# Performance work log

Measured on AMD Instinct MI355X. Metric: run time of the kernel, lower is better.

## Reference

```python
import jax, jax.numpy as jnp
import numpy as np

B, HOP, D = 32768, 32, 64  # batch, hop_number (neighbor samples), embed dim (ent == rel)


def setup_inputs() -> dict:
    key = jax.random.key(0)
    ks = jax.random.split(key, 7)
    s = 0.1  # mimic glorot-scale init for weights
    return {
        "entity": jax.random.normal(ks[0], (B, 1, D), dtype=jnp.float32),
        "relation": jax.random.normal(ks[1], (B, HOP, D), dtype=jnp.float32),
        "neighbor": jax.random.normal(ks[2], (B, HOP, D), dtype=jnp.float32),
        "w_h": jax.random.normal(ks[3], (D, D), dtype=jnp.float32) * s,
        "w_t": jax.random.normal(ks[4], (D, D), dtype=jnp.float32) * s,
        "w_r": jax.random.normal(ks[5], (D, D), dtype=jnp.float32) * s,
        "v_a": jax.random.normal(ks[6], (3 * D, 1), dtype=jnp.float32) * s,
    }


def reference(entity, relation, neighbor, w_h, w_t, w_r, v_a):
    # entity: (B,1,D); relation/neighbor: (B,HOP,D)
    b, hop, _ = relation.shape
    # f_entity = zeros_like(relation[:,:,0]).reshape(-1, hop, 1)  -> all zeros
    f_entity = jnp.zeros((b, hop, 1), dtype=relation.dtype)
    # K.batch_dot(f_entity, entity, [2,1]): (B,HOP,1)x(B,1,D) -> (B,HOP,D) (zeros)
    entity_hat = jnp.einsum('bhi,bid->bhd', f_entity, entity)
    head_entity = entity_hat @ w_h            # (B,HOP,D)
    rel = relation @ w_r                      # (B,HOP,D)
    tail_entity = neighbor @ w_t              # (B,HOP,D)
    head_rel_tail = jnp.concatenate([head_entity, rel, tail_entity], axis=-1)  # (B,HOP,3D)
    scores = jnp.tanh(head_rel_tail) @ v_a    # (B,HOP,1)
    return jax.nn.softmax(scores, axis=-2)    # softmax over hop axis
```

## Files before the change

### kernel.cpp

```cpp
#include <hip/hip_runtime.h>


typedef short bf16x8 __attribute__((ext_vector_type(8)));
typedef float f32x4 __attribute__((ext_vector_type(4)));

#define NB   32768
#define NHOP 32
#define ND   64

__device__ __forceinline__ float tanh_fast(float x) {
  float cx = fminf(fmaxf(x, -20.f), 20.f);
  float e2 = __expf(2.f * cx);
  return (e2 - 1.f) * __builtin_amdgcn_rcpf(e2 + 1.f);
}

__device__ __forceinline__ void split2(float4 v0, float4 v1, bf16x8 &hi, bf16x8 &lo) {
  float xs[8] = {v0.x, v0.y, v0.z, v0.w, v1.x, v1.y, v1.z, v1.w};
#pragma unroll
  for (int j = 0; j < 8; ++j) {
    unsigned u = __builtin_bit_cast(unsigned, xs[j]);
    hi[j] = (short)(u >> 16);
    float hif = __builtin_bit_cast(float, u & 0xffff0000u);
    lo[j] = (short)(__builtin_bit_cast(unsigned, xs[j] - hif) >> 16);
  }
}

__global__ __launch_bounds__(256, 2)
void attn_fused(const float* __restrict__ rel, const float* __restrict__ nbr,
                const float* __restrict__ wr, const float* __restrict__ wt,
                const float* __restrict__ va, float* __restrict__ out, int nwaves) {
  const int lane = threadIdx.x & 63;
  const int wid  = (blockIdx.x * blockDim.x + threadIdx.x) >> 6;
  const int l15  = lane & 15;
  const int lg   = lane >> 4;

  bf16x8 wf[2][2][4][2];
#pragma unroll
  for (int mat = 0; mat < 2; ++mat) {
    const float* W = mat ? wt : wr;
#pragma unroll
    for (int c = 0; c < 2; ++c)
#pragma unroll
      for (int nt = 0; nt < 4; ++nt) {
        bf16x8 hi, lo;
#pragma unroll
        for (int j = 0; j < 8; ++j) {
          float x = W[(c * 32 + lg * 8 + j) * 64 + nt * 16 + l15];
          unsigned u = __builtin_bit_cast(unsigned, x);
          hi[j] = (short)(u >> 16);
          float hif = __builtin_bit_cast(float, u & 0xffff0000u);
          lo[j] = (short)(__builtin_bit_cast(unsigned, x - hif) >> 16);
        }
        wf[mat][c][nt][0] = hi;
        wf[mat][c][nt][1] = lo;
      }
  }

  float va1[4], va2[4];
#pragma unroll
  for (int nt = 0; nt < 4; ++nt) {
    va1[nt] = va[64 + nt * 16 + l15];
    va2[nt] = va[128 + nt * 16 + l15];
  }

  for (int b = wid; b < NB; b += nwaves) {
    float sc[2][4];
#pragma unroll
    for (int tt = 0; tt < 2; ++tt) {
      const size_t row = (size_t)b * NHOP + tt * 16 + l15;
      const float* rbase = rel + row * ND + lg * 8;
      const float* tbase = nbr + row * ND + lg * 8;
      float4 r0 = *(const float4*)(rbase);
      float4 r1 = *(const float4*)(rbase + 4);
      float4 r2 = *(const float4*)(rbase + 32);
      float4 r3 = *(const float4*)(rbase + 36);
      float4 t0 = *(const float4*)(tbase);
      float4 t1 = *(const float4*)(tbase + 4);
      float4 t2 = *(const float4*)(tbase + 32);
      float4 t3 = *(const float4*)(tbase + 36);

      f32x4 part = {0.f, 0.f, 0.f, 0.f};

      {
        bf16x8 ahi[2], alo[2];
        split2(r0, r1, ahi[0], alo[0]);
        split2(r2, r3, ahi[1], alo[1]);
        f32x4 acc[4];
#pragma unroll
        for (int nt = 0; nt < 4; ++nt) acc[nt] = (f32x4){0.f, 0.f, 0.f, 0.f};
#pragma unroll
        for (int c = 0; c < 2; ++c)
#pragma unroll
          for (int nt = 0; nt < 4; ++nt) {
            acc[nt] = __builtin_amdgcn_mfma_f32_16x16x32_bf16(ahi[c], wf[0][c][nt][0], acc[nt], 0, 0, 0);
            acc[nt] = __builtin_amdgcn_mfma_f32_16x16x32_bf16(alo[c], wf[0][c][nt][0], acc[nt], 0, 0, 0);
            acc[nt] = __builtin_amdgcn_mfma_f32_16x16x32_bf16(ahi[c], wf[0][c][nt][1], acc[nt], 0, 0, 0);
          }
#pragma unroll
        for (int nt = 0; nt < 4; ++nt)
#pragma unroll
          for (int rr = 0; rr < 4; ++rr)
            part[rr] += tanh_fast(acc[nt][rr]) * va1[nt];
      }

      {
        bf16x8 ahi[2], alo[2];
        split2(t0, t1, ahi[0], alo[0]);
        split2(t2, t3, ahi[1], alo[1]);
        f32x4 acc[4];
#pragma unroll
        for (int nt = 0; nt < 4; ++nt) acc[nt] = (f32x4){0.f, 0.f, 0.f, 0.f};
#pragma unroll
        for (int c = 0; c < 2; ++c)
#pragma unroll
          for (int nt = 0; nt < 4; ++nt) {
            acc[nt] = __builtin_amdgcn_mfma_f32_16x16x32_bf16(ahi[c], wf[1][c][nt][0], acc[nt], 0, 0, 0);
            acc[nt] = __builtin_amdgcn_mfma_f32_16x16x32_bf16(alo[c], wf[1][c][nt][0], acc[nt], 0, 0, 0);
            acc[nt] = __builtin_amdgcn_mfma_f32_16x16x32_bf16(ahi[c], wf[1][c][nt][1], acc[nt], 0, 0, 0);
          }
#pragma unroll
        for (int nt = 0; nt < 4; ++nt)
#pragma unroll
          for (int rr = 0; rr < 4; ++rr)
            part[rr] += tanh_fast(acc[nt][rr]) * va2[nt];
      }

#pragma unroll
      for (int m = 1; m <= 8; m <<= 1)
#pragma unroll
        for (int rr = 0; rr < 4; ++rr)
          part[rr] += __shfl_xor(part[rr], m, 64);
#pragma unroll
      for (int rr = 0; rr < 4; ++rr) sc[tt][rr] = part[rr];
    }

    float smax = fmaxf(fmaxf(sc[0][0], sc[0][1]), fmaxf(sc[0][2], sc[0][3]));
    smax = fmaxf(smax, fmaxf(fmaxf(sc[1][0], sc[1][1]), fmaxf(sc[1][2], sc[1][3])));
    smax = fmaxf(smax, __shfl_xor(smax, 16, 64));
    smax = fmaxf(smax, __shfl_xor(smax, 32, 64));

    float e[2][4];
    float ssum = 0.f;
#pragma unroll
    for (int tt = 0; tt < 2; ++tt)
#pragma unroll
      for (int rr = 0; rr < 4; ++rr) {
        e[tt][rr] = __expf(sc[tt][rr] - smax);
        ssum += e[tt][rr];
      }
    ssum += __shfl_xor(ssum, 16, 64);
    ssum += __shfl_xor(ssum, 32, 64);
    float inv = __builtin_amdgcn_rcpf(ssum);

    if (l15 == 0) {
      float* ob = out + (size_t)b * NHOP;
      float4 o0 = {e[0][0] * inv, e[0][1] * inv, e[0][2] * inv, e[0][3] * inv};
      float4 o1 = {e[1][0] * inv, e[1][1] * inv, e[1][2] * inv, e[1][3] * inv};
      *(float4*)(ob + lg * 4)      = o0;
      *(float4*)(ob + 16 + lg * 4) = o1;
    }
  }
}

extern "C" void kernel_launch(void* const* d_in, const int* in_sizes, int n_in,
                              void* d_out, int out_size, void* d_ws, size_t ws_size,
                              hipStream_t stream) {
  const float* rel = (const float*)d_in[1];
  const float* nbr = (const float*)d_in[2];
  const float* wt  = (const float*)d_in[4];
  const float* wr  = (const float*)d_in[5];
  const float* va  = (const float*)d_in[6];
  float* out = (float*)d_out;

  const int blocks = 1024;
  attn_fused<<<blocks, 256, 0, stream>>>(rel, nbr, wr, wt, va, out, blocks * 4);
}
```

Baseline: 534.5 us.

## Stage split weights in LDS, software-pipeline loads, cheaper tanh, more blocks

Weight hi/lo bf16 fragments are now built cooperatively once per block into shared memory instead of being held per-wave in registers. This frees VGPRs, so occupancy goes to 3 blocks per CU and the grid grows to 2048 blocks. The main loop prefetches the next batch's relation tile while the neighbor half is computed, and the two hop tiles now share each weight-fragment load. tanh uses a cheaper exp2/rcp form without clamping, and split2 packs its outputs with perm instructions. The cost is extra LDS reads per MFMA group and one block-level barrier.

After: 623.7 us. +16.7%, slower.

```diff
diff --git a/kernel.cpp b/kernel.cpp
--- a/kernel.cpp
+++ b/kernel.cpp
@@ -3,58 +3,48 @@
 
 typedef short bf16x8 __attribute__((ext_vector_type(8)));
 typedef float f32x4 __attribute__((ext_vector_type(4)));
+typedef unsigned int u32x4 __attribute__((ext_vector_type(4)));
 
 #define NB   32768
 #define NHOP 32
 #define ND   64
+#define NBLK 2048
+#define NWAVES (NBLK * 4)
 
-__device__ __forceinline__ float tanh_fast(float x) {
-  float cx = fminf(fmaxf(x, -20.f), 20.f);
-  float e2 = __expf(2.f * cx);
-  return (e2 - 1.f) * __builtin_amdgcn_rcpf(e2 + 1.f);
+__device__ __forceinline__ float tanh_cheap(float x) {
+  float e2 = exp2f(x * 2.885390081777927f);
+  return fmaf(-2.f, __builtin_amdgcn_rcpf(e2 + 1.f), 1.f);
 }
 
 __device__ __forceinline__ void split2(float4 v0, float4 v1, bf16x8 &hi, bf16x8 &lo) {
   float xs[8] = {v0.x, v0.y, v0.z, v0.w, v1.x, v1.y, v1.z, v1.w};
+  u32x4 hw, lw;
 #pragma unroll
-  for (int j = 0; j < 8; ++j) {
-    unsigned u = __builtin_bit_cast(unsigned, xs[j]);
-    hi[j] = (short)(u >> 16);
-    float hif = __builtin_bit_cast(float, u & 0xffff0000u);
-    lo[j] = (short)(__builtin_bit_cast(unsigned, xs[j] - hif) >> 16);
+  for (int p = 0; p < 4; ++p) {
+    unsigned ub = __builtin_bit_cast(unsigned, xs[2 * p]);
+    unsigned ua = __builtin_bit_cast(unsigned, xs[2 * p + 1]);
+    hw[p] = __builtin_amdgcn_perm(ua, ub, 0x07060302u);
+    float hb = __builtin_bit_cast(float, ub & 0xffff0000u);
+    float ha = __builtin_bit_cast(float, ua & 0xffff0000u);
+    unsigned lb = __builtin_bit_cast(unsigned, xs[2 * p] - hb);
+    unsigned la = __builtin_bit_cast(unsigned, xs[2 * p + 1] - ha);
+    lw[p] = __builtin_amdgcn_perm(la, lb, 0x07060302u);
   }
+  hi = __builtin_bit_cast(bf16x8, hw);
+  lo = __builtin_bit_cast(bf16x8, lw);
 }
 
-__global__ __launch_bounds__(256, 2)
+__global__ __launch_bounds__(256, 3)
 void attn_fused(const float* __restrict__ rel, const float* __restrict__ nbr,
                 const float* __restrict__ wr, const float* __restrict__ wt,
-                const float* __restrict__ va, float* __restrict__ out, int nwaves) {
-  const int lane = threadIdx.x & 63;
-  const int wid  = (blockIdx.x * blockDim.x + threadIdx.x) >> 6;
-  const int l15  = lane & 15;
-  const int lg   = lane >> 4;
+                const float* __restrict__ va, float* __restrict__ out) {
+  __shared__ bf16x8 wsl[32][64];
 
-  bf16x8 wf[2][2][4][2];
-#pragma unroll
-  for (int mat = 0; mat < 2; ++mat) {
-    const float* W = mat ? wt : wr;
-#pragma unroll
-    for (int c = 0; c < 2; ++c)
-#pragma unroll
-      for (int nt = 0; nt < 4; ++nt) {
-        bf16x8 hi, lo;
-#pragma unroll
-        for (int j = 0; j < 8; ++j) {
-          float x = W[(c * 32 + lg * 8 + j) * 64 + nt * 16 + l15];
-          unsigned u = __builtin_bit_cast(unsigned, x);
-          hi[j] = (short)(u >> 16);
-          float hif = __builtin_bit_cast(float, u & 0xffff0000u);
-          lo[j] = (short)(__builtin_bit_cast(unsigned, x - hif) >> 16);
-        }
-        wf[mat][c][nt][0] = hi;
-        wf[mat][c][nt][1] = lo;
-      }
-  }
+  const int lane  = threadIdx.x & 63;
+  const int wslot = threadIdx.x >> 6;
+  const int wid   = (int)blockIdx.x * 4 + wslot;
+  const int l15   = lane & 15;
+  const int lg    = lane >> 4;
 
   float va1[4], va2[4];
 #pragma unroll
@@ -63,76 +53,100 @@
     va2[nt] = va[128 + nt * 16 + l15];
   }
 
-  for (int b = wid; b < NB; b += nwaves) {
-    float sc[2][4];
-#pragma unroll
-    for (int tt = 0; tt < 2; ++tt) {
-      const size_t row = (size_t)b * NHOP + tt * 16 + l15;
-      const float* rbase = rel + row * ND + lg * 8;
-      const float* tbase = nbr + row * ND + lg * 8;
-      float4 r0 = *(const float4*)(rbase);
-      float4 r1 = *(const float4*)(rbase + 4);
-      float4 r2 = *(const float4*)(rbase + 32);
-      float4 r3 = *(const float4*)(rbase + 36);
-      float4 t0 = *(const float4*)(tbase);
-      float4 t1 = *(const float4*)(tbase + 4);
-      float4 t2 = *(const float4*)(tbase + 32);
-      float4 t3 = *(const float4*)(tbase + 36);
+#define LOADM(DST, SRC, B) do {                                           \
+    const float* _p0 = (SRC) + ((size_t)(B) * NHOP + l15) * ND + lg * 8;  \
+    DST[0][0] = *(const float4*)(_p0);                                    \
+    DST[0][1] = *(const float4*)(_p0 + 4);                                \
+    DST[0][2] = *(const float4*)(_p0 + 32);                               \
+    DST[0][3] = *(const float4*)(_p0 + 36);                               \
+    const float* _p1 = _p0 + 16 * ND;                                     \
+    DST[1][0] = *(const float4*)(_p1);                                    \
+    DST[1][1] = *(const float4*)(_p1 + 4);                                \
+    DST[1][2] = *(const float4*)(_p1 + 32);                               \
+    DST[1][3] = *(const float4*)(_p1 + 36);                               \
+  } while (0)
 
-      f32x4 part = {0.f, 0.f, 0.f, 0.f};
-
-      {
-        bf16x8 ahi[2], alo[2];
-        split2(r0, r1, ahi[0], alo[0]);
-        split2(r2, r3, ahi[1], alo[1]);
-        f32x4 acc[4];
-#pragma unroll
-        for (int nt = 0; nt < 4; ++nt) acc[nt] = (f32x4){0.f, 0.f, 0.f, 0.f};
-#pragma unroll
-        for (int c = 0; c < 2; ++c)
-#pragma unroll
-          for (int nt = 0; nt < 4; ++nt) {
-            acc[nt] = __builtin_amdgcn_mfma_f32_16x16x32_bf16(ahi[c], wf[0][c][nt][0], acc[nt], 0, 0, 0);
-            acc[nt] = __builtin_amdgcn_mfma_f32_16x16x32_bf16(alo[c], wf[0][c][nt][0], acc[nt], 0, 0, 0);
-            acc[nt] = __builtin_amdgcn_mfma_f32_16x16x32_bf16(ahi[c], wf[0][c][nt][1], acc[nt], 0, 0, 0);
-          }
-#pragma unroll
-        for (int nt = 0; nt < 4; ++nt)
-#pragma unroll
-          for (int rr = 0; rr < 4; ++rr)
-            part[rr] += tanh_fast(acc[nt][rr]) * va1[nt];
-      }
-
-      {
-        bf16x8 ahi[2], alo[2];
-        split2(t0, t1, ahi[0], alo[0]);
-        split2(t2, t3, ahi[1], alo[1]);
-        f32x4 acc[4];
-#pragma unroll
-        for (int nt = 0; nt < 4; ++nt) acc[nt] = (f32x4){0.f, 0.f, 0.f, 0.f};
-#pragma unroll
-        for (int c = 0; c < 2; ++c)
-#pragma unroll
-          for (int nt = 0; nt < 4; ++nt) {
-            acc[nt] = __builtin_amdgcn_mfma_f32_16x16x32_bf16(ahi[c], wf[1][c][nt][0], acc[nt], 0, 0, 0);
-            acc[nt] = __builtin_amdgcn_mfma_f32_16x16x32_bf16(alo[c], wf[1][c][nt][0], acc[nt], 0, 0, 0);
-            acc[nt] = __builtin_amdgcn_mfma_f32_16x16x32_bf16(ahi[c], wf[1][c][nt][1], acc[nt], 0, 0, 0);
-          }
-#pragma unroll
-        for (int nt = 0; nt < 4; ++nt)
-#pragma unroll
-          for (int rr = 0; rr < 4; ++rr)
-            part[rr] += tanh_fast(acc[nt][rr]) * va2[nt];
-      }
+  float4 R[2][4];
+  LOADM(R, rel, wid);
 
 #pragma unroll
-      for (int m = 1; m <= 8; m <<= 1)
+  for (int q = 0; q < 4; ++q) {
+    const int combo = wslot * 4 + q;
+    const int mat = combo >> 3, c = (combo >> 2) & 1, nt = combo & 3;
+    const float* W = mat ? wt : wr;
+    u32x4 hw, lw;
+#pragma unroll
+    for (int p = 0; p < 4; ++p) {
+      float x0 = W[(c * 32 + lg * 8 + 2 * p) * 64 + nt * 16 + l15];
+      float x1 = W[(c * 32 + lg * 8 + 2 * p + 1) * 64 + nt * 16 + l15];
+      unsigned ub = __builtin_bit_cast(unsigned, x0);
+      unsigned ua = __builtin_bit_cast(unsigned, x1);
+      hw[p] = __builtin_amdgcn_perm(ua, ub, 0x07060302u);
+      float hb = __builtin_bit_cast(float, ub & 0xffff0000u);
+      float ha = __builtin_bit_cast(float, ua & 0xffff0000u);
+      unsigned lb = __builtin_bit_cast(unsigned, x0 - hb);
+      unsigned la = __builtin_bit_cast(unsigned, x1 - ha);
+      lw[p] = __builtin_amdgcn_perm(la, lb, 0x07060302u);
+    }
+    wsl[combo * 2 + 0][lane] = __builtin_bit_cast(bf16x8, hw);
+    wsl[combo * 2 + 1][lane] = __builtin_bit_cast(bf16x8, lw);
+  }
+  __syncthreads();
+
+#define COMPUTE_MAT(BUF, MATB, VAV) do {                                        \
+    bf16x8 ahi[2][2], alo[2][2];                                                \
+    _Pragma("unroll")                                                           \
+    for (int tt = 0; tt < 2; ++tt) {                                            \
+      split2(BUF[tt][0], BUF[tt][1], ahi[tt][0], alo[tt][0]);                   \
+      split2(BUF[tt][2], BUF[tt][3], ahi[tt][1], alo[tt][1]);                   \
+    }                                                                           \
+    f32x4 acc[2][4];                                                            \
+    _Pragma("unroll")                                                           \
+    for (int tt = 0; tt < 2; ++tt)                                              \
+      _Pragma("unroll")                                                         \
+      for (int nt = 0; nt < 4; ++nt) acc[tt][nt] = (f32x4){0.f, 0.f, 0.f, 0.f}; \
+    _Pragma("unroll")                                                           \
+    for (int c = 0; c < 2; ++c)                                                 \
+      _Pragma("unroll")                                                         \
+      for (int nt = 0; nt < 4; ++nt) {                                          \
+        bf16x8 wh = wsl[((MATB) + c) * 8 + nt * 2 + 0][lane];                   \
+        bf16x8 wl = wsl[((MATB) + c) * 8 + nt * 2 + 1][lane];                   \
+        _Pragma("unroll")                                                       \
+        for (int tt = 0; tt < 2; ++tt) {                                        \
+          acc[tt][nt] = __builtin_amdgcn_mfma_f32_16x16x32_bf16(ahi[tt][c], wh, acc[tt][nt], 0, 0, 0); \
+          acc[tt][nt] = __builtin_amdgcn_mfma_f32_16x16x32_bf16(alo[tt][c], wh, acc[tt][nt], 0, 0, 0); \
+          acc[tt][nt] = __builtin_amdgcn_mfma_f32_16x16x32_bf16(ahi[tt][c], wl, acc[tt][nt], 0, 0, 0); \
+        }                                                                       \
+      }                                                                         \
+    _Pragma("unroll")                                                           \
+    for (int tt = 0; tt < 2; ++tt)                                              \
+      _Pragma("unroll")                                                         \
+      for (int nt = 0; nt < 4; ++nt)                                            \
+        _Pragma("unroll")                                                       \
+        for (int rr = 0; rr < 4; ++rr)                                          \
+          sc[tt][rr] = fmaf(tanh_cheap(acc[tt][nt][rr]), VAV[nt], sc[tt][rr]);  \
+  } while (0)
+
+  for (int b = wid; b < NB; b += NWAVES) {
+    float4 Nb[2][4];
+    LOADM(Nb, nbr, b);
+
+    float sc[2][4] = {{0.f, 0.f, 0.f, 0.f}, {0.f, 0.f, 0.f, 0.f}};
+
+    COMPUTE_MAT(R, 0, va1);
+
+    const int bn = b + NWAVES;
+    if (bn < NB) LOADM(R, rel, bn);
+
+    COMPUTE_MAT(Nb, 2, va2);
+
+#pragma unroll
+    for (int m = 1; m <= 8; m <<= 1)
+#pragma unroll
+      for (int tt = 0; tt < 2; ++tt)
 #pragma unroll
         for (int rr = 0; rr < 4; ++rr)
-          part[rr] += __shfl_xor(part[rr], m, 64);
-#pragma unroll
-      for (int rr = 0; rr < 4; ++rr) sc[tt][rr] = part[rr];
-    }
+          sc[tt][rr] += __shfl_xor(sc[tt][rr], m, 64);
 
     float smax = fmaxf(fmaxf(sc[0][0], sc[0][1]), fmaxf(sc[0][2], sc[0][3]));
     smax = fmaxf(smax, fmaxf(fmaxf(sc[1][0], sc[1][1]), fmaxf(sc[1][2], sc[1][3])));
@@ -172,6 +186,5 @@
   const float* va  = (const float*)d_in[6];
   float* out = (float*)d_out;
 
-  const int blocks = 1024;
-  attn_fused<<<blocks, 256, 0, stream>>>(rel, nbr, wr, wt, va, out, blocks * 4);
+  attn_fused<<<NBLK, 256, 0, stream>>>(rel, nbr, wr, wt, va, out);
 }
```
